# Optimization experiments

Hardware: AMD Instinct MI355X
Metric: run time of the kernel (lower is better)

## Reference

```python
import jax, jax.numpy as jnp
import numpy as np

B, N, C, H = 16, 288, 32, 32  # batch, nodes, input_size, dg_hidden_size


def setup_inputs() -> dict:
    key = jax.random.key(0)
    ks = jax.random.split(key, 16)
    s = 0.05
    return {
        "inputs": jax.random.normal(ks[0], (B, N, C), jnp.float32),
        "states": jax.random.normal(ks[1], (B, N, H), jnp.float32),
        # rz_gate: Linear(C+H -> 2H), stored [in, out]
        "rz_W": jax.random.normal(ks[2], (C + H, 2 * H), jnp.float32) * s,
        "rz_b": jax.random.normal(ks[3], (2 * H,), jnp.float32) * s,
        # h_candidate: Linear(C+H -> H)
        "hc_W": jax.random.normal(ks[4], (C + H, H), jnp.float32) * s,
        "hc_b": jax.random.normal(ks[5], (H,), jnp.float32) * s,
        # conv (normal_conv): fc2 Linear(2H -> H), fc1 Linear(H -> 1)
        "c1_fc2_W": jax.random.normal(ks[6], (2 * H, H), jnp.float32) * s,
        "c1_fc2_b": jax.random.normal(ks[7], (H,), jnp.float32) * s,
        "c1_fc1_W": jax.random.normal(ks[8], (H, 1), jnp.float32) * s,
        "c1_fc1_b": jax.random.normal(ks[9], (1,), jnp.float32) * s,
        # conv2
        "c2_fc2_W": jax.random.normal(ks[10], (2 * H, H), jnp.float32) * s,
        "c2_fc2_b": jax.random.normal(ks[11], (H,), jnp.float32) * s,
        "c2_fc1_W": jax.random.normal(ks[12], (H, 1), jnp.float32) * s,
        "c2_fc1_b": jax.random.normal(ks[13], (1,), jnp.float32) * s,
    }


def _pair_conv(a, fc2_W, fc2_b, fc1_W, fc1_b):
    # Algebraically equal to fc1(relu(fc2(concat(a_i, a_j)))) without
    # materializing the [B,N,N,2H] concat: split fc2 weights by input half.
    # a: [B,N,H]; fc2_W: [2H,H]
    Hh = a.shape[-1]
    proj_s = a @ fc2_W[:Hh]   # sender half  [B,N,H]
    proj_r = a @ fc2_W[Hh:]   # receiver half [B,N,H]
    h = jax.nn.relu(proj_s[:, :, None, :] + proj_r[:, None, :, :] + fc2_b)  # [B,N,N,H]
    return (h @ fc1_W + fc1_b)[..., 0]  # [B,N,N]


def reference(inputs, states, rz_W, rz_b, hc_W, hc_b,
              c1_fc2_W, c1_fc2_b, c1_fc1_W, c1_fc1_b,
              c2_fc2_W, c2_fc2_b, c2_fc1_W, c2_fc1_b):
    x = jnp.concatenate([inputs, states], axis=-1)          # [B,N,C+H]
    r_z = jax.nn.sigmoid(x @ rz_W + rz_b)                   # [B,N,2H]
    r, z = jnp.split(r_z, 2, axis=-1)
    h_ = jnp.tanh(jnp.concatenate([inputs, r * states], axis=-1) @ hc_W + hc_b)
    new_state = z * states + (1.0 - z) * h_                 # [B,N,H]
    a = jax.nn.relu(new_state)
    support = _pair_conv(a, c1_fc2_W, c1_fc2_b, c1_fc1_W, c1_fc1_b)  # [B,N,N]
    mask = _pair_conv(a, c2_fc2_W, c2_fc2_b, c2_fc1_W, c2_fc1_b)     # [B,N,N]
    support = support * jax.nn.sigmoid(mask)
    return support, new_state
```

## Files before the change

kernel.cpp:

```cpp
#include <hip/hip_runtime.h>
#include <math.h>

#define B_ 16
#define N_ 288
#define C_ 32
#define H_ 32
#define BN_ (B_ * N_)

#define K1_NT 2
#define K1_NODES 8

#define TI 4
#define NTILES (N_ / TI)

typedef float v2f __attribute__((ext_vector_type(2)));

__global__ __launch_bounds__(256) void gru_proj_kernel(
    const float* __restrict__ inputs, const float* __restrict__ states,
    const float* __restrict__ rzW,    const float* __restrict__ rzb,
    const float* __restrict__ hcW,    const float* __restrict__ hcb,
    const float* __restrict__ c1W,    const float* __restrict__ c1b,
    const float* __restrict__ c2W,    const float* __restrict__ c2b,
    float* __restrict__ out_state,
    float* __restrict__ ps1, float* __restrict__ pr1,
    float* __restrict__ ps2, float* __restrict__ pr2)
{
    __shared__ __align__(16) float w_rz[64 * 64];
    __shared__ __align__(16) float w_hc[64 * 32];
    __shared__ __align__(16) float w_c1[64 * 32];
    __shared__ __align__(16) float w_c2[64 * 32];
    __shared__ __align__(16) float x_in[K1_NODES * 32];
    __shared__ __align__(16) float x_st[K1_NODES * 32];
    __shared__ __align__(16) float rs_a[4][K1_NT][32];

    const int tid = threadIdx.x;

    {
        const float4* s4 = (const float4*)rzW;
        float4* d4 = (float4*)w_rz;
        #pragma unroll
        for (int i = 0; i < 4; ++i) d4[tid + i * 256] = s4[tid + i * 256];
        const float4* sh = (const float4*)hcW;
        float4* dh = (float4*)w_hc;
        #pragma unroll
        for (int i = 0; i < 2; ++i) dh[tid + i * 256] = sh[tid + i * 256];
        const float4* sc = (const float4*)c1W;
        float4* dc = (float4*)w_c1;
        #pragma unroll
        for (int i = 0; i < 2; ++i) dc[tid + i * 256] = sc[tid + i * 256];
        #pragma unroll
        for (int i = 0; i < 8; ++i)
            w_c2[tid + i * 256] = c2W[tid + i * 256];
        const int nb = blockIdx.x * K1_NODES * 32;
        x_in[tid] = inputs[nb + tid];
        x_st[tid] = states[nb + tid];
    }
    __syncthreads();

    const int w     = tid >> 6;
    const int lane  = tid & 63;
    const int o     = lane & 31;
    const int half  = lane >> 5;
    const int ln0   = w * K1_NT;
    const int node0 = blockIdx.x * K1_NODES + ln0;

    float acc[K1_NT];
    const float rzbias = rzb[lane];
    acc[0] = rzbias; acc[1] = rzbias;

    #pragma unroll
    for (int q = 0; q < 8; ++q) {
        const float4 xa = *(const float4*)&x_in[(ln0 + 0) * 32 + q * 4];
        const float4 xb = *(const float4*)&x_in[(ln0 + 1) * 32 + q * 4];
        #pragma unroll
        for (int k4 = 0; k4 < 4; ++k4) {
            const float wk = w_rz[(q * 4 + k4) * 64 + lane];
            acc[0] = fmaf(((const float*)&xa)[k4], wk, acc[0]);
            acc[1] = fmaf(((const float*)&xb)[k4], wk, acc[1]);
        }
    }
    #pragma unroll
    for (int q = 0; q < 8; ++q) {
        const float4 xa = *(const float4*)&x_st[(ln0 + 0) * 32 + q * 4];
        const float4 xb = *(const float4*)&x_st[(ln0 + 1) * 32 + q * 4];
        #pragma unroll
        for (int k4 = 0; k4 < 4; ++k4) {
            const float wk = w_rz[(32 + q * 4 + k4) * 64 + lane];
            acc[0] = fmaf(((const float*)&xa)[k4], wk, acc[0]);
            acc[1] = fmaf(((const float*)&xb)[k4], wk, acc[1]);
        }
    }

    float z[K1_NT], st[K1_NT];
    #pragma unroll
    for (int t = 0; t < K1_NT; ++t) {
        const float rzv = 1.0f / (1.0f + __expf(-acc[t]));
        const float r   = __shfl(rzv, o);
        z[t]  = __shfl(rzv, o + 32);
        st[t] = x_st[(ln0 + t) * 32 + o];
        if (lane < 32) rs_a[w][t][o] = r * st[t];
    }

    const float* xs0 = half ? &rs_a[w][0][0] : &x_in[(ln0 + 0) * 32];
    const float* xs1 = half ? &rs_a[w][1][0] : &x_in[(ln0 + 1) * 32];
    float acc2[K1_NT] = {0.0f, 0.0f};
    #pragma unroll
    for (int q = 0; q < 8; ++q) {
        const float4 xa = *(const float4*)&xs0[q * 4];
        const float4 xb = *(const float4*)&xs1[q * 4];
        #pragma unroll
        for (int k4 = 0; k4 < 4; ++k4) {
            const float wk = w_hc[(half * 32 + q * 4 + k4) * 32 + o];
            acc2[0] = fmaf(((const float*)&xa)[k4], wk, acc2[0]);
            acc2[1] = fmaf(((const float*)&xb)[k4], wk, acc2[1]);
        }
    }

    const float hcbias = hcb[o];
    #pragma unroll
    for (int t = 0; t < K1_NT; ++t) {
        acc2[t] += __shfl_xor(acc2[t], 32);
        const float e  = __expf(2.0f * (acc2[t] + hcbias));
        const float hc = 1.0f - 2.0f / (e + 1.0f);
        const float ns = z[t] * st[t] + (1.0f - z[t]) * hc;
        if (lane < 32) out_state[(node0 + t) * H_ + o] = ns;
        if (lane < 32) rs_a[w][t][o] = fmaxf(ns, 0.0f);
    }

    float p1[K1_NT], p2[K1_NT];
    const float b1v = c1b[o], b2v = c2b[o];
    p1[0] = half ? 0.0f : b1v;  p1[1] = p1[0];
    p2[0] = half ? 0.0f : b2v;  p2[1] = p2[0];
    #pragma unroll
    for (int q = 0; q < 8; ++q) {
        const float4 aa = *(const float4*)&rs_a[w][0][q * 4];
        const float4 ab = *(const float4*)&rs_a[w][1][q * 4];
        #pragma unroll
        for (int k4 = 0; k4 < 4; ++k4) {
            const int row  = half * 32 + q * 4 + k4;
            const float w1 = w_c1[row * 32 + o];
            const float w2 = w_c2[row * 32 + o];
            const float a0 = ((const float*)&aa)[k4];
            const float a1 = ((const float*)&ab)[k4];
            p1[0] = fmaf(a0, w1, p1[0]);
            p1[1] = fmaf(a1, w1, p1[1]);
            p2[0] = fmaf(a0, w2, p2[0]);
            p2[1] = fmaf(a1, w2, p2[1]);
        }
    }
    float* d1 = half ? pr1 : ps1;
    float* d2 = half ? pr2 : ps2;
    #pragma unroll
    for (int t = 0; t < K1_NT; ++t) {
        d1[(node0 + t) * H_ + o] = p1[t];
        d2[(node0 + t) * H_ + o] = p2[t];
    }
}

__global__ __launch_bounds__(320) void pair_kernel(
    const float* __restrict__ ps1, const float* __restrict__ pr1,
    const float* __restrict__ ps2, const float* __restrict__ pr2,
    const float* __restrict__ w1g, const float* __restrict__ b1g,
    const float* __restrict__ w2g, const float* __restrict__ b2g,
    float* __restrict__ out)
{
    const int tid = threadIdx.x;
    const int b   = blockIdx.x / NTILES;
    const int i0  = (blockIdx.x % NTILES) * TI;

    __shared__ __align__(16) float s1[TI * 32];
    __shared__ __align__(16) float s2[TI * 32];

    const size_t rowbase = (size_t)(b * N_ + i0) * H_;
    if (tid < TI * 32)            s1[tid]            = ps1[rowbase + tid];
    else if (tid < 2 * TI * 32)   s2[tid - TI * 32]  = ps2[rowbase + (tid - TI * 32)];
    __syncthreads();

    const int j = tid;
    if (j < N_) {
        const v2f zero = {0.0f, 0.0f};
        float acc1[TI];

        {
            const float4* prp = (const float4*)(pr1 + (size_t)(b * N_ + j) * H_);
            v2f p0[8], p1v[8], w0[8], w1v[8];
            #pragma unroll
            for (int c = 0; c < 8; ++c) {
                const float4 pv = prp[c];
                p0[c]  = (v2f){pv.x, pv.y};
                p1v[c] = (v2f){pv.z, pv.w};
                w0[c]  = (v2f){w1g[4 * c + 0], w1g[4 * c + 1]};
                w1v[c] = (v2f){w1g[4 * c + 2], w1g[4 * c + 3]};
            }
            const float b1 = b1g[0];
            #pragma unroll
            for (int ii = 0; ii < TI; ++ii) {
                v2f aA = {b1, 0.0f}, aB = zero;
                #pragma unroll
                for (int c = 0; c < 8; ++c) {
                    const float4 sv = *(const float4*)&s1[ii * 32 + c * 4];
                    v2f u0 = (v2f){sv.x, sv.y} + p0[c];
                    v2f u1 = (v2f){sv.z, sv.w} + p1v[c];
                    u0 = __builtin_elementwise_max(u0, zero);
                    u1 = __builtin_elementwise_max(u1, zero);
                    aA = u0 * w0[c] + aA;
                    aB = u1 * w1v[c] + aB;
                }
                acc1[ii] = aA.x + aA.y + aB.x + aB.y;
            }
        }

        {
            const float4* prp = (const float4*)(pr2 + (size_t)(b * N_ + j) * H_);
            v2f p0[8], p1v[8], w0[8], w1v[8];
            #pragma unroll
            for (int c = 0; c < 8; ++c) {
                const float4 pv = prp[c];
                p0[c]  = (v2f){pv.x, pv.y};
                p1v[c] = (v2f){pv.z, pv.w};
                w0[c]  = (v2f){w2g[4 * c + 0], w2g[4 * c + 1]};
                w1v[c] = (v2f){w2g[4 * c + 2], w2g[4 * c + 3]};
            }
            const float b2 = b2g[0];
            float* orow = out + (size_t)(b * N_ + i0) * N_ + j;
            #pragma unroll
            for (int ii = 0; ii < TI; ++ii) {
                v2f aA = {b2, 0.0f}, aB = zero;
                #pragma unroll
                for (int c = 0; c < 8; ++c) {
                    const float4 sv = *(const float4*)&s2[ii * 32 + c * 4];
                    v2f u0 = (v2f){sv.x, sv.y} + p0[c];
                    v2f u1 = (v2f){sv.z, sv.w} + p1v[c];
                    u0 = __builtin_elementwise_max(u0, zero);
                    u1 = __builtin_elementwise_max(u1, zero);
                    aA = u0 * w0[c] + aA;
                    aB = u1 * w1v[c] + aB;
                }
                const float m   = aA.x + aA.y + aB.x + aB.y;
                const float sig = 1.0f / (1.0f + __expf(-m));
                orow[(size_t)ii * N_] = acc1[ii] * sig;
            }
        }
    }
}

extern "C" void kernel_launch(void* const* d_in, const int* in_sizes, int n_in,
                              void* d_out, int out_size, void* d_ws, size_t ws_size,
                              hipStream_t stream) {
    const float* inputs = (const float*)d_in[0];
    const float* states = (const float*)d_in[1];
    const float* rzW    = (const float*)d_in[2];
    const float* rzb    = (const float*)d_in[3];
    const float* hcW    = (const float*)d_in[4];
    const float* hcb    = (const float*)d_in[5];
    const float* c1W    = (const float*)d_in[6];
    const float* c1b    = (const float*)d_in[7];
    const float* c1w1   = (const float*)d_in[8];
    const float* c1b1   = (const float*)d_in[9];
    const float* c2W    = (const float*)d_in[10];
    const float* c2b    = (const float*)d_in[11];
    const float* c2w1   = (const float*)d_in[12];
    const float* c2b1   = (const float*)d_in[13];

    float* out_support = (float*)d_out;
    float* out_state   = out_support + (size_t)BN_ * N_;

    float* ws  = (float*)d_ws;
    float* ps1 = ws;
    float* pr1 = ws + 1 * (size_t)BN_ * H_;
    float* ps2 = ws + 2 * (size_t)BN_ * H_;
    float* pr2 = ws + 3 * (size_t)BN_ * H_;

    gru_proj_kernel<<<BN_ / K1_NODES, 256, 0, stream>>>(
        inputs, states, rzW, rzb, hcW, hcb, c1W, c1b, c2W, c2b,
        out_state, ps1, pr1, ps2, pr2);

    pair_kernel<<<B_ * NTILES, 320, 0, stream>>>(
        ps1, pr1, ps2, pr2, c1w1, c1b1, c2w1, c2b1, out_support);
}
```

Measured before the change: 29.36 us.

## Shrink GRU kernel to one wave, read weights from global, transpose receiver projections

The first kernel now launches 64-thread blocks that each handle 4 nodes. It drops the large shared-memory weight staging and reads weights and activations directly from global memory, relying on the cache. The receiver-side projections are written in a [8][BN][4] float4-blocked transposed layout, so the pair kernel's per-thread float4 loads across neighbouring j become coalesced instead of strided by 128 bytes. The trade-off is more global and L2 traffic for weights in the first kernel, plus more, smaller blocks.

```diff
diff --git a/kernel.cpp b/kernel.cpp
--- a/kernel.cpp
+++ b/kernel.cpp
@@ -6,160 +6,149 @@
 #define C_ 32
 #define H_ 32
 #define BN_ (B_ * N_)
-
-#define K1_NT 2
-#define K1_NODES 8
+#define NT 4
 
 #define TI 4
 #define NTILES (N_ / TI)
 
 typedef float v2f __attribute__((ext_vector_type(2)));
 
-__global__ __launch_bounds__(256) void gru_proj_kernel(
+__global__ __launch_bounds__(64) void gru_proj_kernel(
     const float* __restrict__ inputs, const float* __restrict__ states,
     const float* __restrict__ rzW,    const float* __restrict__ rzb,
     const float* __restrict__ hcW,    const float* __restrict__ hcb,
     const float* __restrict__ c1W,    const float* __restrict__ c1b,
     const float* __restrict__ c2W,    const float* __restrict__ c2b,
     float* __restrict__ out_state,
-    float* __restrict__ ps1, float* __restrict__ pr1,
-    float* __restrict__ ps2, float* __restrict__ pr2)
+    float* __restrict__ ps1, float* __restrict__ ps2,
+    float* __restrict__ pr1T, float* __restrict__ pr2T)
 {
-    __shared__ __align__(16) float w_rz[64 * 64];
-    __shared__ __align__(16) float w_hc[64 * 32];
-    __shared__ __align__(16) float w_c1[64 * 32];
-    __shared__ __align__(16) float w_c2[64 * 32];
-    __shared__ __align__(16) float x_in[K1_NODES * 32];
-    __shared__ __align__(16) float x_st[K1_NODES * 32];
-    __shared__ __align__(16) float rs_a[4][K1_NT][32];
-
-    const int tid = threadIdx.x;
-
-    {
-        const float4* s4 = (const float4*)rzW;
-        float4* d4 = (float4*)w_rz;
-        #pragma unroll
-        for (int i = 0; i < 4; ++i) d4[tid + i * 256] = s4[tid + i * 256];
-        const float4* sh = (const float4*)hcW;
-        float4* dh = (float4*)w_hc;
-        #pragma unroll
-        for (int i = 0; i < 2; ++i) dh[tid + i * 256] = sh[tid + i * 256];
-        const float4* sc = (const float4*)c1W;
-        float4* dc = (float4*)w_c1;
-        #pragma unroll
-        for (int i = 0; i < 2; ++i) dc[tid + i * 256] = sc[tid + i * 256];
-        #pragma unroll
-        for (int i = 0; i < 8; ++i)
-            w_c2[tid + i * 256] = c2W[tid + i * 256];
-        const int nb = blockIdx.x * K1_NODES * 32;
-        x_in[tid] = inputs[nb + tid];
-        x_st[tid] = states[nb + tid];
-    }
-    __syncthreads();
-
-    const int w     = tid >> 6;
-    const int lane  = tid & 63;
+    const int lane  = threadIdx.x;
     const int o     = lane & 31;
     const int half  = lane >> 5;
-    const int ln0   = w * K1_NT;
-    const int node0 = blockIdx.x * K1_NODES + ln0;
-
-    float acc[K1_NT];
+    const int node0 = blockIdx.x * NT;
+
+    __shared__ __align__(16) float xh_sh[NT][64];
+    __shared__ __align__(16) float a_sh[NT][32];
+
+    if (!half) {
+        #pragma unroll
+        for (int t = 0; t < NT; ++t)
+            xh_sh[t][o] = inputs[(node0 + t) * C_ + o];
+    }
+
+    float acc_i[NT], acc_s[NT];
     const float rzbias = rzb[lane];
-    acc[0] = rzbias; acc[1] = rzbias;
+    #pragma unroll
+    for (int t = 0; t < NT; ++t) { acc_i[t] = rzbias; acc_s[t] = 0.0f; }
 
     #pragma unroll
     for (int q = 0; q < 8; ++q) {
-        const float4 xa = *(const float4*)&x_in[(ln0 + 0) * 32 + q * 4];
-        const float4 xb = *(const float4*)&x_in[(ln0 + 1) * 32 + q * 4];
+        float4 xi[NT], xs[NT];
+        #pragma unroll
+        for (int t = 0; t < NT; ++t) {
+            xi[t] = *(const float4*)&inputs[(node0 + t) * C_ + q * 4];
+            xs[t] = *(const float4*)&states[(node0 + t) * H_ + q * 4];
+        }
         #pragma unroll
         for (int k4 = 0; k4 < 4; ++k4) {
-            const float wk = w_rz[(q * 4 + k4) * 64 + lane];
-            acc[0] = fmaf(((const float*)&xa)[k4], wk, acc[0]);
-            acc[1] = fmaf(((const float*)&xb)[k4], wk, acc[1]);
-        }
-    }
-    #pragma unroll
-    for (int q = 0; q < 8; ++q) {
-        const float4 xa = *(const float4*)&x_st[(ln0 + 0) * 32 + q * 4];
-        const float4 xb = *(const float4*)&x_st[(ln0 + 1) * 32 + q * 4];
-        #pragma unroll
-        for (int k4 = 0; k4 < 4; ++k4) {
-            const float wk = w_rz[(32 + q * 4 + k4) * 64 + lane];
-            acc[0] = fmaf(((const float*)&xa)[k4], wk, acc[0]);
-            acc[1] = fmaf(((const float*)&xb)[k4], wk, acc[1]);
-        }
-    }
-
-    float z[K1_NT], st[K1_NT];
-    #pragma unroll
-    for (int t = 0; t < K1_NT; ++t) {
-        const float rzv = 1.0f / (1.0f + __expf(-acc[t]));
+            const float wi = rzW[(q * 4 + k4) * 64 + lane];
+            const float ws = rzW[(32 + q * 4 + k4) * 64 + lane];
+            #pragma unroll
+            for (int t = 0; t < NT; ++t) {
+                acc_i[t] = fmaf(((const float*)&xi[t])[k4], wi, acc_i[t]);
+                acc_s[t] = fmaf(((const float*)&xs[t])[k4], ws, acc_s[t]);
+            }
+        }
+    }
+
+    float z[NT], st[NT];
+    #pragma unroll
+    for (int t = 0; t < NT; ++t) {
+        const float rzv = 1.0f / (1.0f + __expf(-(acc_i[t] + acc_s[t])));
         const float r   = __shfl(rzv, o);
         z[t]  = __shfl(rzv, o + 32);
-        st[t] = x_st[(ln0 + t) * 32 + o];
-        if (lane < 32) rs_a[w][t][o] = r * st[t];
-    }
-
-    const float* xs0 = half ? &rs_a[w][0][0] : &x_in[(ln0 + 0) * 32];
-    const float* xs1 = half ? &rs_a[w][1][0] : &x_in[(ln0 + 1) * 32];
-    float acc2[K1_NT] = {0.0f, 0.0f};
+        st[t] = states[(node0 + t) * H_ + o];
+        if (half) xh_sh[t][32 + o] = r * st[t];
+    }
+    __syncthreads();
+
+    float acc2[NT] = {0.0f, 0.0f, 0.0f, 0.0f};
     #pragma unroll
     for (int q = 0; q < 8; ++q) {
-        const float4 xa = *(const float4*)&xs0[q * 4];
-        const float4 xb = *(const float4*)&xs1[q * 4];
+        float4 xh[NT];
+        #pragma unroll
+        for (int t = 0; t < NT; ++t)
+            xh[t] = *(const float4*)&xh_sh[t][half * 32 + q * 4];
         #pragma unroll
         for (int k4 = 0; k4 < 4; ++k4) {
-            const float wk = w_hc[(half * 32 + q * 4 + k4) * 32 + o];
-            acc2[0] = fmaf(((const float*)&xa)[k4], wk, acc2[0]);
-            acc2[1] = fmaf(((const float*)&xb)[k4], wk, acc2[1]);
+            const float wk = hcW[(half * 32 + q * 4 + k4) * 32 + o];
+            #pragma unroll
+            for (int t = 0; t < NT; ++t)
+                acc2[t] = fmaf(((const float*)&xh[t])[k4], wk, acc2[t]);
         }
     }
 
     const float hcbias = hcb[o];
     #pragma unroll
-    for (int t = 0; t < K1_NT; ++t) {
+    for (int t = 0; t < NT; ++t) {
         acc2[t] += __shfl_xor(acc2[t], 32);
         const float e  = __expf(2.0f * (acc2[t] + hcbias));
         const float hc = 1.0f - 2.0f / (e + 1.0f);
         const float ns = z[t] * st[t] + (1.0f - z[t]) * hc;
-        if (lane < 32) out_state[(node0 + t) * H_ + o] = ns;
-        if (lane < 32) rs_a[w][t][o] = fmaxf(ns, 0.0f);
-    }
-
-    float p1[K1_NT], p2[K1_NT];
+        if (!half) {
+            out_state[(node0 + t) * H_ + o] = ns;
+            a_sh[t][o] = fmaxf(ns, 0.0f);
+        }
+    }
+    __syncthreads();
+
+    float p1[NT], p2[NT];
     const float b1v = c1b[o], b2v = c2b[o];
-    p1[0] = half ? 0.0f : b1v;  p1[1] = p1[0];
-    p2[0] = half ? 0.0f : b2v;  p2[1] = p2[0];
+    #pragma unroll
+    for (int t = 0; t < NT; ++t) {
+        p1[t] = half ? 0.0f : b1v;
+        p2[t] = half ? 0.0f : b2v;
+    }
+    const int rb = half * 32;
     #pragma unroll
     for (int q = 0; q < 8; ++q) {
-        const float4 aa = *(const float4*)&rs_a[w][0][q * 4];
-        const float4 ab = *(const float4*)&rs_a[w][1][q * 4];
+        float4 aq[NT];
+        #pragma unroll
+        for (int t = 0; t < NT; ++t)
+            aq[t] = *(const float4*)&a_sh[t][q * 4];
         #pragma unroll
         for (int k4 = 0; k4 < 4; ++k4) {
-            const int row  = half * 32 + q * 4 + k4;
-            const float w1 = w_c1[row * 32 + o];
-            const float w2 = w_c2[row * 32 + o];
-            const float a0 = ((const float*)&aa)[k4];
-            const float a1 = ((const float*)&ab)[k4];
-            p1[0] = fmaf(a0, w1, p1[0]);
-            p1[1] = fmaf(a1, w1, p1[1]);
-            p2[0] = fmaf(a0, w2, p2[0]);
-            p2[1] = fmaf(a1, w2, p2[1]);
-        }
-    }
-    float* d1 = half ? pr1 : ps1;
-    float* d2 = half ? pr2 : ps2;
-    #pragma unroll
-    for (int t = 0; t < K1_NT; ++t) {
-        d1[(node0 + t) * H_ + o] = p1[t];
-        d2[(node0 + t) * H_ + o] = p2[t];
+            const int row  = rb + q * 4 + k4;
+            const float w1 = c1W[row * 32 + o];
+            const float w2 = c2W[row * 32 + o];
+            #pragma unroll
+            for (int t = 0; t < NT; ++t) {
+                const float av = ((const float*)&aq[t])[k4];
+                p1[t] = fmaf(av, w1, p1[t]);
+                p2[t] = fmaf(av, w2, p2[t]);
+            }
+        }
+    }
+    if (!half) {
+        #pragma unroll
+        for (int t = 0; t < NT; ++t) {
+            ps1[(node0 + t) * H_ + o] = p1[t];
+            ps2[(node0 + t) * H_ + o] = p2[t];
+        }
+    } else {
+        const int qo = o >> 2, ro = o & 3;
+        #pragma unroll
+        for (int t = 0; t < NT; ++t) {
+            pr1T[((size_t)qo * BN_ + node0 + t) * 4 + ro] = p1[t];
+            pr2T[((size_t)qo * BN_ + node0 + t) * 4 + ro] = p2[t];
+        }
     }
 }
 
 __global__ __launch_bounds__(320) void pair_kernel(
-    const float* __restrict__ ps1, const float* __restrict__ pr1,
-    const float* __restrict__ ps2, const float* __restrict__ pr2,
+    const float* __restrict__ ps1, const float* __restrict__ pr1T,
+    const float* __restrict__ ps2, const float* __restrict__ pr2T,
     const float* __restrict__ w1g, const float* __restrict__ b1g,
     const float* __restrict__ w2g, const float* __restrict__ b2g,
     float* __restrict__ out)
@@ -172,21 +161,22 @@
     __shared__ __align__(16) float s2[TI * 32];
 
     const size_t rowbase = (size_t)(b * N_ + i0) * H_;
-    if (tid < TI * 32)            s1[tid]            = ps1[rowbase + tid];
-    else if (tid < 2 * TI * 32)   s2[tid - TI * 32]  = ps2[rowbase + (tid - TI * 32)];
+    if (tid < TI * 32)            s1[tid]           = ps1[rowbase + tid];
+    else if (tid < 2 * TI * 32)   s2[tid - TI * 32] = ps2[rowbase + (tid - TI * 32)];
     __syncthreads();
 
     const int j = tid;
     if (j < N_) {
+        const size_t jj = (size_t)(b * N_ + j);
         const v2f zero = {0.0f, 0.0f};
         float acc1[TI];
 
         {
-            const float4* prp = (const float4*)(pr1 + (size_t)(b * N_ + j) * H_);
+            const float4* prp = (const float4*)pr1T;
             v2f p0[8], p1v[8], w0[8], w1v[8];
             #pragma unroll
             for (int c = 0; c < 8; ++c) {
-                const float4 pv = prp[c];
+                const float4 pv = prp[(size_t)c * BN_ + jj];
                 p0[c]  = (v2f){pv.x, pv.y};
                 p1v[c] = (v2f){pv.z, pv.w};
                 w0[c]  = (v2f){w1g[4 * c + 0], w1g[4 * c + 1]};
@@ -211,11 +201,11 @@
         }
 
         {
-            const float4* prp = (const float4*)(pr2 + (size_t)(b * N_ + j) * H_);
+            const float4* prp = (const float4*)pr2T;
             v2f p0[8], p1v[8], w0[8], w1v[8];
             #pragma unroll
             for (int c = 0; c < 8; ++c) {
-                const float4 pv = prp[c];
+                const float4 pv = prp[(size_t)c * BN_ + jj];
                 p0[c]  = (v2f){pv.x, pv.y};
                 p1v[c] = (v2f){pv.z, pv.w};
                 w0[c]  = (v2f){w2g[4 * c + 0], w2g[4 * c + 1]};
@@ -265,16 +255,16 @@
     float* out_support = (float*)d_out;
     float* out_state   = out_support + (size_t)BN_ * N_;
 
-    float* ws  = (float*)d_ws;
-    float* ps1 = ws;
-    float* pr1 = ws + 1 * (size_t)BN_ * H_;
-    float* ps2 = ws + 2 * (size_t)BN_ * H_;
-    float* pr2 = ws + 3 * (size_t)BN_ * H_;
-
-    gru_proj_kernel<<<BN_ / K1_NODES, 256, 0, stream>>>(
+    float* ws   = (float*)d_ws;
+    float* ps1  = ws;
+    float* ps2  = ws + 1 * (size_t)BN_ * H_;
+    float* pr1T = ws + 2 * (size_t)BN_ * H_;
+    float* pr2T = ws + 3 * (size_t)BN_ * H_;
+
+    gru_proj_kernel<<<BN_ / NT, 64, 0, stream>>>(
         inputs, states, rzW, rzb, hcW, hcb, c1W, c1b, c2W, c2b,
-        out_state, ps1, pr1, ps2, pr2);
+        out_state, ps1, ps2, pr1T, pr2T);
 
     pair_kernel<<<B_ * NTILES, 320, 0, stream>>>(
-        ps1, pr1, ps2, pr2, c1w1, c1b1, c2w1, c2b1, out_support);
+        ps1, pr1T, ps2, pr2T, c1w1, c1b1, c2w1, c2b1, out_support);
 }
```

Result: faster. 28.00 us (-4.6%).
